# Performance work log

Hardware: AMD Instinct MI355X
Metric: run time of the kernel (lower is better)

Reference implementation:

```python
import jax, jax.numpy as jnp
import numpy as np

N_NODES = 100000
N_EDGES = 3200000
N_FEAT = 500
N_HID = 256
N_CLASS = 40


def spmm(edge_row, edge_col, edge_val, x, num_nodes):
    # out[i] = sum_{e: row[e]==i} val[e] * x[col[e]]
    msgs = edge_val[:, None] * x[edge_col]          # [E, F] gather + scale
    return jax.ops.segment_sum(msgs, edge_row, num_segments=num_nodes)


def setup_inputs() -> dict:
    key = jax.random.key(0)
    k1, k2, k3, k4, k5, k6, k7, k8 = jax.random.split(key, 8)
    features = jax.random.normal(k1, (N_NODES, N_FEAT), dtype=jnp.float32)
    edge_row = jax.random.randint(k2, (N_EDGES,), 0, N_NODES, dtype=jnp.int32)
    edge_col = jax.random.randint(k3, (N_EDGES,), 0, N_NODES, dtype=jnp.int32)
    edge_val = jax.random.uniform(k4, (N_EDGES,), dtype=jnp.float32)
    # Xavier-uniform linear weights, zero biases (as in reset_parameters)
    lim1 = float(np.sqrt(6.0 / (N_FEAT + N_HID)))
    W1 = jax.random.uniform(k5, (N_FEAT, N_HID), minval=-lim1, maxval=lim1, dtype=jnp.float32)
    b1 = jnp.zeros((N_HID,), dtype=jnp.float32)
    lim2 = float(np.sqrt(6.0 / (N_HID + N_CLASS)))
    W2 = jax.random.uniform(k6, (N_HID, N_CLASS), minval=-lim2, maxval=lim2, dtype=jnp.float32)
    b2 = jnp.zeros((N_CLASS,), dtype=jnp.float32)
    return {
        "features": features,
        "edge_row": edge_row,
        "edge_col": edge_col,
        "edge_val": edge_val,
        "W1": W1, "b1": b1, "W2": W2, "b2": b2,
    }


def reference(features, edge_row, edge_col, edge_val, W1, b1, W2, b2):
    # Layer 1: linear -> spmm -> relu   (eval mode: dropout is identity)
    h = features @ W1 + b1                          # [N, nhid]
    h = spmm(edge_row, edge_col, edge_val, h, N_NODES)
    h = jax.nn.relu(h)
    # Layer 2: linear -> spmm
    o = h @ W2 + b2                                 # [N, nclass]
    o = spmm(edge_row, edge_col, edge_val, o, N_NODES)
    return jax.nn.log_softmax(o, axis=1)
```

## Files before the change

### kernel.cpp

```cpp
#include <hip/hip_runtime.h>
#include <hip/hip_bf16.h>
#include <math.h>

#define N_NODES 100000
#define N_FEAT 500
#define N_HID 256
#define N_CLASS 40

typedef float f32x4 __attribute__((ext_vector_type(4)));
typedef float f32x2 __attribute__((ext_vector_type(2)));
typedef int i32x4 __attribute__((ext_vector_type(4)));
typedef unsigned int u32x4 __attribute__((ext_vector_type(4)));
typedef short short8 __attribute__((ext_vector_type(8)));
typedef unsigned short u16x8 __attribute__((ext_vector_type(8)));

__device__ __forceinline__ float b2f(unsigned short u) {
  union { unsigned int i; float f; } c; c.i = ((unsigned int)u) << 16; return c.f;
}
__device__ __forceinline__ unsigned short f2bu(float x) {
  __hip_bfloat16 b = __float2bfloat16(x);
  union { __hip_bfloat16 b; unsigned short u; } c; c.b = b; return c.u;
}
__device__ __forceinline__ float decode_val(unsigned int p) {
  union { unsigned int i; float f; } c; c.i = (p & 0x7FFFu) << 17; return c.f;
}
__device__ __forceinline__ unsigned char f2fp8(float x) {
  return (unsigned char)(__builtin_amdgcn_cvt_pk_fp8_f32(x, x, 0, false) & 0xFF);
}
__device__ __forceinline__ void gload_lds16(const void* gptr, void* lptr) {
  __builtin_amdgcn_global_load_lds(
      (const __attribute__((address_space(1))) unsigned int*)gptr,
      (__attribute__((address_space(3))) unsigned int*)lptr, 16, 0, 0);
}

__global__ __launch_bounds__(256) void prep_kernel(
    const float* __restrict__ W1, unsigned short* __restrict__ Bsw,
    const int* __restrict__ er, const int* __restrict__ ec,
    const float* __restrict__ ev, int* __restrict__ cnt,
    unsigned int* __restrict__ cvps, int E) {
  if (blockIdx.x < 64) {
    int t = blockIdx.x * 256 + threadIdx.x;
    int col = t >> 6, ch = t & 63;
    int g = ch >> 3, c = ch & 7;
    int c_src = c ^ (col & 7);
    int k = g * 64 + c_src * 8;
    u16x8 o;
#pragma unroll
    for (int j = 0; j < 8; j++) {
      int kk = k + j;
      o[j] = (kk < N_FEAT) ? f2bu(W1[(size_t)kk * N_HID + col]) : (unsigned short)0;
    }
    *(u16x8*)(Bsw + (size_t)col * 512 + g * 64 + c * 8) = o;
  }
  int nv = E >> 2;
  int t = blockIdx.x * 256 + threadIdx.x;
  int nthr = gridDim.x * 256;
  const i32x4* er4 = (const i32x4*)er;
  const i32x4* ec4 = (const i32x4*)ec;
  const f32x4* ev4 = (const f32x4*)ev;
  for (int i = t; i < nv; i += nthr) {
    i32x4 r = __builtin_nontemporal_load(&er4[i]);
    i32x4 c = __builtin_nontemporal_load(&ec4[i]);
    f32x4 v = __builtin_nontemporal_load(&ev4[i]);
    atomicAdd(&cnt[r.x], 1);
    atomicAdd(&cnt[r.y], 1);
    atomicAdd(&cnt[r.z], 1);
    atomicAdd(&cnt[r.w], 1);
    u32x4 pk;
    pk.x = ((unsigned int)c.x << 15) | ((unsigned int)f2bu(v.x) >> 1);
    pk.y = ((unsigned int)c.y << 15) | ((unsigned int)f2bu(v.y) >> 1);
    pk.z = ((unsigned int)c.z << 15) | ((unsigned int)f2bu(v.z) >> 1);
    pk.w = ((unsigned int)c.w << 15) | ((unsigned int)f2bu(v.w) >> 1);
    __builtin_nontemporal_store(pk, (u32x4*)(cvps + 4 * (size_t)i));
  }
  int tail = nv << 2;
  if (blockIdx.x == 0 && threadIdx.x < E - tail) {
    int i = tail + threadIdx.x;
    atomicAdd(&cnt[er[i]], 1);
    cvps[i] = ((unsigned int)ec[i] << 15) | ((unsigned int)f2bu(ev[i]) >> 1);
  }
}

__global__ __launch_bounds__(256) void gemm1_mfma(
    const float* __restrict__ A, const unsigned short* __restrict__ Bsw,
    const float* __restrict__ b1, unsigned char* __restrict__ H, int M) {
  __shared__ __align__(16) char smem[36864];
  char* sA = smem;
  char* sB = smem + 4096;
  int tid = threadIdx.x;
  int lane = tid & 63, w = tid >> 6;
  int wc = w;
  int bm = blockIdx.x * 32;

  f32x4 acc[2][4];
#pragma unroll
  for (int m = 0; m < 2; m++)
#pragma unroll
    for (int n = 0; n < 4; n++) acc[m][n] = (f32x4)0.f;

  for (int s = 0; s < 8; s++) {
    int k0 = s * 64;
#pragma unroll
    for (int i = 0; i < 2; i++) {
      int f4 = i * 256 + tid;
      int row = f4 >> 4, cidx = f4 & 15;
      int grow = bm + row;
      int k = k0 + cidx * 4;
      float4 v = make_float4(0.f, 0.f, 0.f, 0.f);
      if (grow < M && k < N_FEAT) v = *(const float4*)(A + (size_t)grow * N_FEAT + k);
      ushort4 u;
      u.x = f2bu(v.x); u.y = f2bu(v.y); u.z = f2bu(v.z); u.w = f2bu(v.w);
      int chunk = cidx >> 1, sub = cidx & 1;
      int byte = row * 128 + (((chunk ^ (row & 7))) << 4) + (sub << 3);
      *(ushort4*)(sA + byte) = u;
    }
#pragma unroll
    for (int j = 0; j < 8; j++) {
      int base = j * 4096 + w * 1024;
      int L = base + lane * 16;
      int col = L >> 7, c = (L >> 4) & 7;
      const char* g = (const char*)Bsw + (size_t)col * 1024 + s * 128 + c * 16;
      gload_lds16(g, sB + base);
    }
    __syncthreads();
#pragma unroll
    for (int kk = 0; kk < 2; kk++) {
      int cw = kk * 4 + (lane >> 4);
      short8 af[2], bg[4];
#pragma unroll
      for (int m = 0; m < 2; m++) {
        int ar = m * 16 + (lane & 15);
        af[m] = *(const short8*)(sA + ar * 128 + ((cw ^ (ar & 7)) << 4));
      }
#pragma unroll
      for (int n = 0; n < 4; n++) {
        int bc = wc * 64 + n * 16 + (lane & 15);
        bg[n] = *(const short8*)(sB + bc * 128 + ((cw ^ (bc & 7)) << 4));
      }
#pragma unroll
      for (int m = 0; m < 2; m++)
#pragma unroll
        for (int n = 0; n < 4; n++)
          acc[m][n] = __builtin_amdgcn_mfma_f32_16x16x32_bf16(af[m], bg[n], acc[m][n], 0, 0, 0);
    }
    __syncthreads();
  }

  float bias[4];
#pragma unroll
  for (int n = 0; n < 4; n++) bias[n] = b1[wc * 64 + n * 16 + (lane & 15)];
#pragma unroll
  for (int m = 0; m < 2; m++) {
#pragma unroll
    for (int r = 0; r < 4; r++) {
      int row = bm + m * 16 + ((lane >> 4) << 2) + r;
      if (row < M) {
#pragma unroll
        for (int n = 0; n < 4; n++) {
          int col = wc * 64 + n * 16 + (lane & 15);
          H[(size_t)row * N_HID + col] = f2fp8(acc[m][n][r] + bias[n]);
        }
      }
    }
  }
}

__global__ __launch_bounds__(1024) void scan1_kernel(
    int* __restrict__ cnt, int* __restrict__ bsum, int n) {
  __shared__ int wsum[16];
  int tid = threadIdx.x, lane = tid & 63, wid = tid >> 6;
  int i = blockIdx.x * 1024 + tid;
  int v = (i < n) ? cnt[i] : 0;
  int x = v;
#pragma unroll
  for (int off = 1; off < 64; off <<= 1) {
    int t = __shfl_up(x, off);
    if (lane >= off) x += t;
  }
  if (lane == 63) wsum[wid] = x;
  __syncthreads();
  if (tid < 16) {
    int ws = wsum[tid];
#pragma unroll
    for (int off = 1; off < 16; off <<= 1) {
      int t = __shfl_up(ws, off);
      if (tid >= off) ws += t;
    }
    wsum[tid] = ws;
  }
  __syncthreads();
  int excl = (wid ? wsum[wid - 1] : 0) + x - v;
  if (i < n) cnt[i] = excl;
  if (tid == 0) bsum[blockIdx.x] = wsum[15];
}

__global__ __launch_bounds__(64) void scan2_kernel(
    int* __restrict__ bsum, int* __restrict__ row_ptr, int nb, int n) {
  int lane = threadIdx.x;
  int carry = 0;
  for (int base = 0; base < nb; base += 64) {
    int i = base + lane;
    int v = (i < nb) ? bsum[i] : 0;
    int x = v;
#pragma unroll
    for (int off = 1; off < 64; off <<= 1) {
      int t = __shfl_up(x, off);
      if (lane >= off) x += t;
    }
    if (i < nb) bsum[i] = carry + x - v;
    carry += __shfl(x, 63);
  }
  if (lane == 0) row_ptr[n] = carry;
}

__global__ __launch_bounds__(256) void scan3_kernel(
    int* __restrict__ cnt, const int* __restrict__ bsum,
    int* __restrict__ row_ptr, int n) {
  int i = blockIdx.x * 256 + threadIdx.x;
  if (i >= n) return;
  int v = cnt[i] + bsum[i >> 10];
  cnt[i] = v;
  row_ptr[i] = v;
}

__global__ __launch_bounds__(256) void scatter_kernel(
    const int* __restrict__ er, const unsigned int* __restrict__ cvps,
    int* __restrict__ cursor, unsigned int* __restrict__ cvp, int E) {
  int s = blockIdx.x & 3;
  int g = blockIdx.x >> 2;
  int ngrp = gridDim.x >> 2;
  int nv = E >> 2;
  const i32x4* er4 = (const i32x4*)er;
  const u32x4* cv4 = (const u32x4*)cvps;
  for (int i = g * 256 + threadIdx.x; i < nv; i += ngrp * 256) {
    i32x4 r = __builtin_nontemporal_load(&er4[i]);
    u32x4 p = __builtin_nontemporal_load(&cv4[i]);
    if (((r.x >> 9) & 3) == s) cvp[atomicAdd(&cursor[r.x], 1)] = p.x;
    if (((r.y >> 9) & 3) == s) cvp[atomicAdd(&cursor[r.y], 1)] = p.y;
    if (((r.z >> 9) & 3) == s) cvp[atomicAdd(&cursor[r.z], 1)] = p.z;
    if (((r.w >> 9) & 3) == s) cvp[atomicAdd(&cursor[r.w], 1)] = p.w;
  }
  int tail = nv << 2;
  if (blockIdx.x == 0 && threadIdx.x < E - tail) {
    int i = tail + threadIdx.x;
    cvp[atomicAdd(&cursor[er[i]], 1)] = cvps[i];
  }
}

__global__ __launch_bounds__(256) void spmm_fp8(
    const int* __restrict__ row_ptr, const unsigned int* __restrict__ cvp,
    const unsigned char* __restrict__ X, unsigned short* __restrict__ Y, int M) {
  int wave = (blockIdx.x * 256 + threadIdx.x) >> 6;
  int lane = threadIdx.x & 63;
  if (wave >= M) return;
  int start = row_ptr[wave], end = row_ptr[wave + 1];
  int qf = lane >> 4, fl = lane & 15;
  f32x4 a0 = (f32x4)0.f, a1 = (f32x4)0.f, a2 = (f32x4)0.f, a3 = (f32x4)0.f;
  const unsigned char* Xf = X + fl * 16;
#pragma unroll 2
  for (int e = start; e < end; e += 4) {
    int ei = e + qf;
    unsigned int p = (ei < end) ? cvp[ei] : 0u;
    float val = decode_val(p);
    size_t col = (size_t)(p >> 15);
    u32x4 d = *(const u32x4*)(Xf + col * N_HID);
    f32x2 f0 = __builtin_amdgcn_cvt_pk_f32_fp8(d.x, false);
    f32x2 f1 = __builtin_amdgcn_cvt_pk_f32_fp8(d.x, true);
    f32x2 f2 = __builtin_amdgcn_cvt_pk_f32_fp8(d.y, false);
    f32x2 f3 = __builtin_amdgcn_cvt_pk_f32_fp8(d.y, true);
    f32x2 f4 = __builtin_amdgcn_cvt_pk_f32_fp8(d.z, false);
    f32x2 f5 = __builtin_amdgcn_cvt_pk_f32_fp8(d.z, true);
    f32x2 f6 = __builtin_amdgcn_cvt_pk_f32_fp8(d.w, false);
    f32x2 f7 = __builtin_amdgcn_cvt_pk_f32_fp8(d.w, true);
    a0.x = fmaf(val, f0.x, a0.x); a0.y = fmaf(val, f0.y, a0.y);
    a0.z = fmaf(val, f1.x, a0.z); a0.w = fmaf(val, f1.y, a0.w);
    a1.x = fmaf(val, f2.x, a1.x); a1.y = fmaf(val, f2.y, a1.y);
    a1.z = fmaf(val, f3.x, a1.z); a1.w = fmaf(val, f3.y, a1.w);
    a2.x = fmaf(val, f4.x, a2.x); a2.y = fmaf(val, f4.y, a2.y);
    a2.z = fmaf(val, f5.x, a2.z); a2.w = fmaf(val, f5.y, a2.w);
    a3.x = fmaf(val, f6.x, a3.x); a3.y = fmaf(val, f6.y, a3.y);
    a3.z = fmaf(val, f7.x, a3.z); a3.w = fmaf(val, f7.y, a3.w);
  }
#define RED2(v) v += __shfl_xor(v, 16); v += __shfl_xor(v, 32);
  RED2(a0.x) RED2(a0.y) RED2(a0.z) RED2(a0.w)
  RED2(a1.x) RED2(a1.y) RED2(a1.z) RED2(a1.w)
  RED2(a2.x) RED2(a2.y) RED2(a2.z) RED2(a2.w)
  RED2(a3.x) RED2(a3.y) RED2(a3.z) RED2(a3.w)
#undef RED2
  if (qf == 0) {
    u16x8 o;
    o[0] = f2bu(fmaxf(a0.x, 0.f)); o[1] = f2bu(fmaxf(a0.y, 0.f));
    o[2] = f2bu(fmaxf(a0.z, 0.f)); o[3] = f2bu(fmaxf(a0.w, 0.f));
    o[4] = f2bu(fmaxf(a1.x, 0.f)); o[5] = f2bu(fmaxf(a1.y, 0.f));
    o[6] = f2bu(fmaxf(a1.z, 0.f)); o[7] = f2bu(fmaxf(a1.w, 0.f));
    *(u16x8*)(Y + (size_t)wave * N_HID + fl * 16) = o;
    o[0] = f2bu(fmaxf(a2.x, 0.f)); o[1] = f2bu(fmaxf(a2.y, 0.f));
    o[2] = f2bu(fmaxf(a2.z, 0.f)); o[3] = f2bu(fmaxf(a2.w, 0.f));
    o[4] = f2bu(fmaxf(a3.x, 0.f)); o[5] = f2bu(fmaxf(a3.y, 0.f));
    o[6] = f2bu(fmaxf(a3.z, 0.f)); o[7] = f2bu(fmaxf(a3.w, 0.f));
    *(u16x8*)(Y + (size_t)wave * N_HID + fl * 16 + 8) = o;
  }
}

__global__ __launch_bounds__(256) void gemm2_kernel(
    const unsigned short* __restrict__ H, const float* __restrict__ W2,
    const float* __restrict__ b2, unsigned short* __restrict__ O, int M) {
  __shared__ float Ws[N_HID * N_CLASS];
  __shared__ float sb2[N_CLASS];
  int tid = threadIdx.x;
  for (int i = tid; i < N_HID * N_CLASS; i += 256) Ws[i] = W2[i];
  if (tid < N_CLASS) sb2[tid] = b2[tid];
  __syncthreads();
  int r0 = (blockIdx.x * 256 + tid) * 2;
  if (r0 >= M) return;
  int r1 = r0 + 1;
  bool has1 = r1 < M;
  float acc0[N_CLASS], acc1[N_CLASS];
#pragma unroll
  for (int n = 0; n < N_CLASS; n++) { acc0[n] = sb2[n]; acc1[n] = sb2[n]; }
  const unsigned short* h0 = H + (size_t)r0 * N_HID;
  const unsigned short* h1 = H + (size_t)(has1 ? r1 : r0) * N_HID;
  for (int k0 = 0; k0 < N_HID; k0 += 8) {
    u16x8 va = *(const u16x8*)(h0 + k0);
    u16x8 vb = *(const u16x8*)(h1 + k0);
#pragma unroll
    for (int j = 0; j < 8; j++) {
      float a0 = b2f(va[j]), a1 = b2f(vb[j]);
      const float* wrow = &Ws[(k0 + j) * N_CLASS];
#pragma unroll
      for (int n = 0; n < N_CLASS; n++) {
        float wv = wrow[n];
        acc0[n] = fmaf(a0, wv, acc0[n]);
        acc1[n] = fmaf(a1, wv, acc1[n]);
      }
    }
  }
  unsigned short* o0 = O + (size_t)r0 * N_CLASS;
#pragma unroll
  for (int n = 0; n < N_CLASS; n += 4) {
    ushort4 p;
    p.x = f2bu(acc0[n]); p.y = f2bu(acc0[n + 1]);
    p.z = f2bu(acc0[n + 2]); p.w = f2bu(acc0[n + 3]);
    *(ushort4*)(o0 + n) = p;
  }
  if (has1) {
    unsigned short* o1 = O + (size_t)r1 * N_CLASS;
#pragma unroll
    for (int n = 0; n < N_CLASS; n += 4) {
      ushort4 p;
      p.x = f2bu(acc1[n]); p.y = f2bu(acc1[n + 1]);
      p.z = f2bu(acc1[n + 2]); p.w = f2bu(acc1[n + 3]);
      *(ushort4*)(o1 + n) = p;
    }
  }
}

__global__ __launch_bounds__(256) void spmm_csr_40_lsm(
    const int* __restrict__ row_ptr, const unsigned int* __restrict__ cvp,
    const unsigned short* __restrict__ X, float* __restrict__ Out, int M) {
  int wave = (blockIdx.x * 256 + threadIdx.x) >> 6;
  int lane = threadIdx.x & 63;
  if (wave >= M) return;
  int start = row_ptr[wave], end = row_ptr[wave + 1];
  bool act = lane < N_CLASS;
  int ln = act ? lane : 0;
  const unsigned short* Xc = X + ln;
  float acc = 0.f;
  int e = start;
  for (; e + 4 <= end; e += 4) {
    unsigned int p0 = cvp[e], p1 = cvp[e + 1], p2 = cvp[e + 2], p3 = cvp[e + 3];
    unsigned short x0 = Xc[(size_t)(p0 >> 15) * N_CLASS];
    unsigned short x1 = Xc[(size_t)(p1 >> 15) * N_CLASS];
    unsigned short x2 = Xc[(size_t)(p2 >> 15) * N_CLASS];
    unsigned short x3 = Xc[(size_t)(p3 >> 15) * N_CLASS];
    acc = fmaf(decode_val(p0), b2f(x0), acc);
    acc = fmaf(decode_val(p1), b2f(x1), acc);
    acc = fmaf(decode_val(p2), b2f(x2), acc);
    acc = fmaf(decode_val(p3), b2f(x3), acc);
  }
  for (; e < end; e++) {
    unsigned int p0 = cvp[e];
    acc = fmaf(decode_val(p0), b2f(Xc[(size_t)(p0 >> 15) * N_CLASS]), acc);
  }
  float mv = act ? acc : -INFINITY;
#pragma unroll
  for (int off = 32; off; off >>= 1) mv = fmaxf(mv, __shfl_xor(mv, off));
  float ex = act ? expf(acc - mv) : 0.f;
  float s = ex;
#pragma unroll
  for (int off = 32; off; off >>= 1) s += __shfl_xor(s, off);
  float lse = mv + logf(s);
  if (act) Out[(size_t)wave * N_CLASS + lane] = acc - lse;
}

extern "C" void kernel_launch(void* const* d_in, const int* in_sizes, int n_in,
                              void* d_out, int out_size, void* d_ws, size_t ws_size,
                              hipStream_t stream) {
  const float* feat = (const float*)d_in[0];
  const int* er     = (const int*)d_in[1];
  const int* ec     = (const int*)d_in[2];
  const float* ev   = (const float*)d_in[3];
  const float* W1   = (const float*)d_in[4];
  const float* b1   = (const float*)d_in[5];
  const float* W2   = (const float*)d_in[6];
  const float* b2   = (const float*)d_in[7];
  float* out = (float*)d_out;
  const int M = N_NODES;
  const int E = in_sizes[1];

  char* ws = (char*)d_ws;
  unsigned char* h      = (unsigned char*)(ws);
  unsigned short* hpost = (unsigned short*)(ws + 25600000);
  unsigned short* o     = (unsigned short*)(ws + 76800000);
  int* row_ptr          = (int*)(ws + 84800000);
  int* cursor           = (int*)(ws + 85200016);
  int* bsum             = (int*)(ws + 85600016);
  unsigned int* cvp     = (unsigned int*)(ws + 85600528);
  unsigned int* cvps    = (unsigned int*)(ws + 98400528);
  unsigned short* W1Tsw = (unsigned short*)(ws + 111200528);

  const int NB1 = (M + 1023) / 1024;

  (void)hipMemsetAsync(cursor, 0, (size_t)M * sizeof(int), stream);
  prep_kernel<<<1024, 256, 0, stream>>>(W1, W1Tsw, er, ec, ev, cursor, cvps, E);
  scan1_kernel<<<NB1, 1024, 0, stream>>>(cursor, bsum, M);
  scan2_kernel<<<1, 64, 0, stream>>>(bsum, row_ptr, NB1, M);
  scan3_kernel<<<(M + 255) / 256, 256, 0, stream>>>(cursor, bsum, row_ptr, M);
  scatter_kernel<<<2048, 256, 0, stream>>>(er, cvps, cursor, cvp, E);
  gemm1_mfma<<<(M + 31) / 32, 256, 0, stream>>>(feat, W1Tsw, b1, h, M);
  spmm_fp8<<<(M + 3) / 4, 256, 0, stream>>>(row_ptr, cvp, h, hpost, M);
  gemm2_kernel<<<(M + 511) / 512, 256, 0, stream>>>(hpost, W2, b2, o, M);
  spmm_csr_40_lsm<<<(M + 3) / 4, 256, 0, stream>>>(row_ptr, cvp, o, out, M);
}
```

Baseline: 650.2 us.

## Prefetch next edge in SpMM and halve scatter row-partition passes

The fp8 SpMM loop now loads the next packed column/value word one iteration ahead, so the index load overlaps the dependent feature gather. The scatter kernel splits rows into 2 partitions instead of 4, so each edge chunk is read fewer times, and it writes the scattered entries with nontemporal stores. The coarser partition may spread atomic traffic less evenly, and the prefetch adds a register per lane and one extra speculative load per row.

```diff
diff --git a/kernel.cpp b/kernel.cpp
--- a/kernel.cpp
+++ b/kernel.cpp
@@ -226,19 +226,31 @@
 __global__ __launch_bounds__(256) void scatter_kernel(
     const int* __restrict__ er, const unsigned int* __restrict__ cvps,
     int* __restrict__ cursor, unsigned int* __restrict__ cvp, int E) {
-  int s = blockIdx.x & 3;
-  int g = blockIdx.x >> 2;
-  int ngrp = gridDim.x >> 2;
+  int s = blockIdx.x & 1;
+  int g = blockIdx.x >> 1;
+  int ngrp = gridDim.x >> 1;
   int nv = E >> 2;
   const i32x4* er4 = (const i32x4*)er;
   const u32x4* cv4 = (const u32x4*)cvps;
   for (int i = g * 256 + threadIdx.x; i < nv; i += ngrp * 256) {
     i32x4 r = __builtin_nontemporal_load(&er4[i]);
     u32x4 p = __builtin_nontemporal_load(&cv4[i]);
-    if (((r.x >> 9) & 3) == s) cvp[atomicAdd(&cursor[r.x], 1)] = p.x;
-    if (((r.y >> 9) & 3) == s) cvp[atomicAdd(&cursor[r.y], 1)] = p.y;
-    if (((r.z >> 9) & 3) == s) cvp[atomicAdd(&cursor[r.z], 1)] = p.z;
-    if (((r.w >> 9) & 3) == s) cvp[atomicAdd(&cursor[r.w], 1)] = p.w;
+    if (((r.x >> 9) & 1) == s) {
+      int pos = atomicAdd(&cursor[r.x], 1);
+      __builtin_nontemporal_store(p.x, &cvp[pos]);
+    }
+    if (((r.y >> 9) & 1) == s) {
+      int pos = atomicAdd(&cursor[r.y], 1);
+      __builtin_nontemporal_store(p.y, &cvp[pos]);
+    }
+    if (((r.z >> 9) & 1) == s) {
+      int pos = atomicAdd(&cursor[r.z], 1);
+      __builtin_nontemporal_store(p.z, &cvp[pos]);
+    }
+    if (((r.w >> 9) & 1) == s) {
+      int pos = atomicAdd(&cursor[r.w], 1);
+      __builtin_nontemporal_store(p.w, &cvp[pos]);
+    }
   }
   int tail = nv << 2;
   if (blockIdx.x == 0 && threadIdx.x < E - tail) {
@@ -257,12 +269,17 @@
   int qf = lane >> 4, fl = lane & 15;
   f32x4 a0 = (f32x4)0.f, a1 = (f32x4)0.f, a2 = (f32x4)0.f, a3 = (f32x4)0.f;
   const unsigned char* Xf = X + fl * 16;
+  unsigned int pcur;
+  {
+    int ei = start + qf;
+    pcur = (ei < end) ? cvp[ei] : 0u;
+  }
 #pragma unroll 2
   for (int e = start; e < end; e += 4) {
-    int ei = e + qf;
-    unsigned int p = (ei < end) ? cvp[ei] : 0u;
-    float val = decode_val(p);
-    size_t col = (size_t)(p >> 15);
+    int en = e + 4 + qf;
+    unsigned int pnext = (en < end) ? cvp[en] : 0u;
+    float val = decode_val(pcur);
+    size_t col = (size_t)(pcur >> 15);
     u32x4 d = *(const u32x4*)(Xf + col * N_HID);
     f32x2 f0 = __builtin_amdgcn_cvt_pk_f32_fp8(d.x, false);
     f32x2 f1 = __builtin_amdgcn_cvt_pk_f32_fp8(d.x, true);
@@ -280,6 +297,7 @@
     a2.z = fmaf(val, f5.x, a2.z); a2.w = fmaf(val, f5.y, a2.w);
     a3.x = fmaf(val, f6.x, a3.x); a3.y = fmaf(val, f6.y, a3.y);
     a3.z = fmaf(val, f7.x, a3.z); a3.w = fmaf(val, f7.y, a3.w);
+    pcur = pnext;
   }
 #define RED2(v) v += __shfl_xor(v, 16); v += __shfl_xor(v, 32);
   RED2(a0.x) RED2(a0.y) RED2(a0.z) RED2(a0.w)
```

Measured after the change: 730.0 us. +12.3%, slower.
